# Optimization experiments

Hardware: AMD Instinct MI355X
Metric: run time of the kernel (lower is better)

The kernel has to match this reference:

```python
import jax, jax.numpy as jnp
import numpy as np

EPS = 1e-5

def binarize(x):
    # straight-through-estimator sign binarization (identity gradient),
    # matching the torch .data-mutation trick in BinarizeConv2d/BinarizeLinear
    return x + jax.lax.stop_gradient(jnp.sign(x) - x)

def conv3x3(x, w, b):
    # NCHW conv, stride 1, padding 1, binarized weights, float bias
    y = jax.lax.conv_general_dilated(x, binarize(w), window_strides=(1, 1),
                                     padding=((1, 1), (1, 1)),
                                     dimension_numbers=('NCHW', 'OIHW', 'NCHW'))
    return y + b[None, :, None, None]

def maxpool2(x):
    return jax.lax.reduce_window(x, -jnp.inf, jax.lax.max,
                                 (1, 1, 2, 2), (1, 1, 2, 2), 'VALID')

def bn2d(x, g, b):
    # training-mode batchnorm (batch statistics)
    m = jnp.mean(x, axis=(0, 2, 3), keepdims=True)
    v = jnp.var(x, axis=(0, 2, 3), keepdims=True)
    return (x - m) * jax.lax.rsqrt(v + EPS) * g[None, :, None, None] + b[None, :, None, None]

def bn1d(x, g, b):
    m = jnp.mean(x, axis=0)
    v = jnp.var(x, axis=0)
    return (x - m) * jax.lax.rsqrt(v + EPS) * g + b

def htanh(x):
    return jnp.clip(x, -1.0, 1.0)


def setup_inputs() -> dict:
    key = jax.random.key(0)
    ks = jax.random.split(key, 16)
    B = 1024
    inp = {
        'x':   jax.random.normal(ks[0], (B, 1, 28, 28), jnp.float32),
        'w1':  jax.random.normal(ks[1], (48, 1, 3, 3), jnp.float32) * 0.1,
        'b1':  jnp.zeros((48,), jnp.float32),
        'g1':  jnp.ones((48,), jnp.float32),  'be1': jnp.zeros((48,), jnp.float32),
        'w2':  jax.random.normal(ks[2], (128, 48, 3, 3), jnp.float32) * 0.05,
        'b2':  jnp.zeros((128,), jnp.float32),
        'g2':  jnp.ones((128,), jnp.float32), 'be2': jnp.zeros((128,), jnp.float32),
        'w3':  jax.random.normal(ks[3], (256, 128, 3, 3), jnp.float32) * 0.03,
        'b3':  jnp.zeros((256,), jnp.float32),
        'g3':  jnp.ones((256,), jnp.float32), 'be3': jnp.zeros((256,), jnp.float32),
        'wf1': jax.random.normal(ks[4], (2048, 256 * 7 * 7), jnp.float32) * 0.01,
        'bf1': jnp.zeros((2048,), jnp.float32),
        'g4':  jnp.ones((2048,), jnp.float32), 'be4': jnp.zeros((2048,), jnp.float32),
        'wf2': jax.random.normal(ks[5], (10, 2048), jnp.float32) * 0.02,
        'bf2': jnp.zeros((10,), jnp.float32),
    }
    return inp


def reference(x, w1, b1, g1, be1, w2, b2, g2, be2, w3, b3, g3, be3,
              wf1, bf1, g4, be4, wf2, bf2):
    # features
    h = conv3x3(binarize(x), w1, b1)          # [B,48,28,28] (input binarized: C=1 != 3)
    h = maxpool2(h)                            # [B,48,14,14]
    h = htanh(bn2d(h, g1, be1))
    h = conv3x3(binarize(h), w2, b2)          # [B,128,14,14]
    h = htanh(bn2d(h, g2, be2))
    h = conv3x3(binarize(h), w3, b3)          # [B,256,14,14]
    h = maxpool2(h)                            # [B,256,7,7]
    h = htanh(bn2d(h, g3, be3))
    # classifier
    h = h.reshape(-1, 256 * 7 * 7)
    h = binarize(h) @ binarize(wf1).T + bf1    # [B,2048]
    h = htanh(bn1d(h, g4, be4))
    # Dropout(0.5) is identity in eval mode
    h = h @ wf2.T + bf2                        # [B,10]
    return jax.nn.log_softmax(h, axis=1)
```

## Files before the change

### kernel.cpp

```cpp
#include <hip/hip_runtime.h>
#include <math.h>

typedef __attribute__((ext_vector_type(8))) short short8;
typedef __attribute__((ext_vector_type(4))) float f32x4;
typedef unsigned short ushort_t;

#define B_    1024
#define EPSV  1e-5

__device__ __forceinline__ float sgn(float v){ return (v>0.f)?1.f:((v<0.f)?-1.f:0.f); }
__device__ __forceinline__ ushort_t sgnbits(float v){ return (v>0.f)?(ushort_t)0x3F80:((v<0.f)?(ushort_t)0xBF80:(ushort_t)0); }

#define SWZW(o,c) ( ((o)<<6) ^ ((((c) ^ ((o)&7)) & 7) << 4) )
#define SWZF(o,c) ( ((o)<<7) + ((((c) ^ ((o)&7)) & 7) << 4) )

__global__ __launch_bounds__(256) void k_conv1_pool(const float* __restrict__ x,
                                                    const float* __restrict__ w1,
                                                    float* __restrict__ p1){
  int idx = blockIdx.x*256 + threadIdx.x;
  if (idx >= B_*196*64) return;
  int c = idx & 63;
  int p = (idx >> 6) % 196;
  int b = (idx >> 6) / 196;
  if (c >= 48){ p1[idx] = 0.f; return; }
  int y = p/14, xq = p - y*14;
  const float* xb = x + (size_t)b*784;
  float w[9];
#pragma unroll
  for (int k=0;k<9;k++) w[k] = sgn(w1[c*9+k]);
  float sx[4][4];
#pragma unroll
  for (int dy=0; dy<4; dy++){
    int iy = 2*y-1+dy;
#pragma unroll
    for (int dx=0; dx<4; dx++){
      int ix = 2*xq-1+dx;
      sx[dy][dx] = (iy>=0 && iy<28 && ix>=0 && ix<28) ? sgn(xb[iy*28+ix]) : 0.f;
    }
  }
  float best = -1e30f;
#pragma unroll
  for (int py=0;py<2;py++)
#pragma unroll
    for (int px=0;px<2;px++){
      float acc = 0.f;
#pragma unroll
      for (int ky=0;ky<3;ky++)
#pragma unroll
        for (int kx=0;kx<3;kx++)
          acc += sx[py+ky][px+kx]*w[ky*3+kx];
      best = fmaxf(best, acc);
    }
  p1[idx] = best;
}

__global__ __launch_bounds__(256) void k_stats_cl64(const float* __restrict__ src,
                                                    double* __restrict__ sum,
                                                    double* __restrict__ sumsq,
                                                    long rows){
  int c = threadIdx.x & 63, sl = threadIdx.x >> 6;
  double a=0.0, q=0.0;
  long stride = (long)gridDim.y*4;
  for (long r = (long)blockIdx.y*4 + sl; r < rows; r += stride){
    double v = (double)src[r*64 + c];
    a += v; q += v*v;
  }
  __shared__ double sA[256], sQd[256];
  sA[threadIdx.x]=a; sQd[threadIdx.x]=q;
  __syncthreads();
  if (threadIdx.x < 64){
    a = sA[threadIdx.x] + sA[threadIdx.x+64] + sA[threadIdx.x+128] + sA[threadIdx.x+192];
    q = sQd[threadIdx.x] + sQd[threadIdx.x+64] + sQd[threadIdx.x+128] + sQd[threadIdx.x+192];
    atomicAdd(&sum[c], a); atomicAdd(&sumsq[c], q);
  }
}

__global__ __launch_bounds__(256) void k_reduce_stats(const float* __restrict__ pS,
                                                      const float* __restrict__ pQ,
                                                      double* __restrict__ sum,
                                                      double* __restrict__ sumsq,
                                                      int C, int nPart){
  int c = blockIdx.x*256 + threadIdx.x;
  if (c >= C) return;
  int per = (nPart + gridDim.y - 1)/gridDim.y;
  int p0 = blockIdx.y*per, p1 = p0+per; if (p1 > nPart) p1 = nPart;
  double a=0.0, q=0.0;
  for (int p = p0; p < p1; ++p){
    a += (double)pS[(size_t)p*C + c];
    q += (double)pQ[(size_t)p*C + c];
  }
  atomicAdd(&sum[c], a); atomicAdd(&sumsq[c], q);
}

__global__ void k_bnparams(const double* __restrict__ sum, const double* __restrict__ sumsq,
                           const float* __restrict__ g, const float* __restrict__ be,
                           float* __restrict__ scale, float* __restrict__ shift,
                           int C, int validC, double invN){
  int c = blockIdx.x*blockDim.x + threadIdx.x;
  if (c >= C) return;
  if (c >= validC){ scale[c]=0.f; shift[c]=0.f; return; }
  double m   = sum[c]*invN;
  double var = sumsq[c]*invN - m*m;
  double s   = (double)g[c] / sqrt(var + EPSV);
  scale[c] = (float)s;
  shift[c] = (float)((double)be[c] - m*s);
}

__global__ __launch_bounds__(256) void k_norm_sign(const float* __restrict__ src,
                                                   ushort_t* __restrict__ dst,
                                                   const float* __restrict__ scale,
                                                   const float* __restrict__ shift,
                                                   int C, int S, int total){
  int i = blockIdx.x*256 + threadIdx.x;
  if (i >= total) return;
  int c = (i / S) % C;
  float v = fmaf(src[i], scale[c], shift[c]);
  dst[i] = sgnbits(v);
}

__global__ __launch_bounds__(256) void k_norm_htanh(float* __restrict__ buf,
                                                    const float* __restrict__ scale,
                                                    const float* __restrict__ shift,
                                                    int C, int total){
  int i = blockIdx.x*256 + threadIdx.x;
  if (i >= total) return;
  int c = i % C;
  float v = fmaf(buf[i], scale[c], shift[c]);
  buf[i] = fminf(fmaxf(v,-1.f),1.f);
}

__global__ __launch_bounds__(256) void k_prep_w2(const float* __restrict__ w2, ushort_t* __restrict__ out){
  int idx = blockIdx.x*256 + threadIdx.x;
  if (idx >= 128*576) return;
  int oc = idx / 576, r = idx - oc*576;
  int kk = r >> 6, ic = r & 63;
  out[idx] = (ic < 48) ? sgnbits(w2[oc*432 + ic*9 + kk]) : (ushort_t)0;
}
__global__ __launch_bounds__(256) void k_prep_w3(const float* __restrict__ w3, ushort_t* __restrict__ out){
  int idx = blockIdx.x*256 + threadIdx.x;
  if (idx >= 256*1152) return;
  int oc = idx / 1152, r = idx - oc*1152;
  int kk = r >> 7, ic = r & 127;
  out[idx] = sgnbits(w3[oc*1152 + ic*9 + kk]);
}
__global__ __launch_bounds__(256) void k_prep_wf1(const float* __restrict__ wf1, ushort_t* __restrict__ out){
  int idx = blockIdx.x*256 + threadIdx.x;
  if (idx >= 2048*12544/4) return;
  const float4 v = *reinterpret_cast<const float4*>(&wf1[(size_t)idx*4]);
  ushort4 o;
  o.x = sgnbits(v.x); o.y = sgnbits(v.y); o.z = sgnbits(v.z); o.w = sgnbits(v.w);
  *reinterpret_cast<ushort4*>(&out[(size_t)idx*4]) = o;
}

__global__ __launch_bounds__(256,2) void k_conv2_mfma(const ushort_t* __restrict__ a1,
                                                      const ushort_t* __restrict__ w2b,
                                                      float* __restrict__ c2,
                                                      float* __restrict__ pS,
                                                      float* __restrict__ pQ){
  __shared__ ushort_t sIn[256*64];
  __shared__ char     sWb[2][8192];
  __shared__ float    sRS[128], sRQ[128];
  int b = blockIdx.x, tid = threadIdx.x;
  {
    const uint4* src4 = reinterpret_cast<const uint4*>(a1 + (size_t)b*196*64);
    for (int i = tid; i < 2048; i += 256){
      int px = i >> 3, ch = i & 7;
      int py = px >> 4, pxx = px & 15;
      uint4 v = make_uint4(0u,0u,0u,0u);
      if (py>=1 && py<=14 && pxx>=1 && pxx<=14)
        v = src4[((py-1)*14 + (pxx-1))*8 + ch];
      *reinterpret_cast<uint4*>(&sIn[px*64 + ((ch ^ (px & 7))<<3)]) = v;
    }
  }
  if (tid < 128){ sRS[tid]=0.f; sRQ[tid]=0.f; }
  const uint4* gW = reinterpret_cast<const uint4*>(w2b);
  int cS = tid & 3, rS = (tid >> 2)*2;
  {
    uint4 v0 = gW[(size_t)rS*72 + cS];
    uint4 v1 = gW[(size_t)(rS+1)*72 + cS];
    *reinterpret_cast<uint4*>(&sWb[0][SWZW(rS,  cS)]) = v0;
    *reinterpret_cast<uint4*>(&sWb[0][SWZW(rS+1,cS)]) = v1;
  }
  __syncthreads();
  int lane = tid & 63, wave = tid >> 6;
  int rA = lane & 15, kch = lane >> 4;
  f32x4 acc[4][8];
#pragma unroll
  for (int t=0;t<4;t++)
#pragma unroll
    for (int n=0;n<8;n++) acc[t][n] = (f32x4){0.f,0.f,0.f,0.f};

  for (int s = 0; s < 18; ++s){
    int cur = s & 1;
    uint4 w0, w1;
    if (s < 17){
      w0 = gW[(size_t)rS*72 + (s+1)*4 + cS];
      w1 = gW[(size_t)(rS+1)*72 + (s+1)*4 + cS];
    }
    short8 bF[8];
#pragma unroll
    for (int n=0;n<8;n++){
      int o = n*16 + rA;
      bF[n] = *reinterpret_cast<const short8*>(&sWb[cur][SWZW(o, kch)]);
    }
    int kk9 = s >> 1;
    int ky = kk9/3, kx = kk9 - ky*3;
    int chbase = ((s & 1) << 2) + kch;
#pragma unroll
    for (int t=0;t<4;t++){
      int m = t*4 + wave;
      if (m < 13){
        int r = m*16 + rA;
        int rc = r < 196 ? r : 195;
        int y = rc/14, x = rc - y*14;
        int px = (y+ky)*16 + (x+kx);
        short8 aF = *reinterpret_cast<const short8*>(&sIn[px*64 + ((chbase ^ (px&7))<<3)]);
#pragma unroll
        for (int n=0;n<8;n++)
          acc[t][n] = __builtin_amdgcn_mfma_f32_16x16x32_bf16(aF, bF[n], acc[t][n], 0,0,0);
      }
    }
    if (s < 17){
      *reinterpret_cast<uint4*>(&sWb[cur^1][SWZW(rS,  cS)]) = w0;
      *reinterpret_cast<uint4*>(&sWb[cur^1][SWZW(rS+1,cS)]) = w1;
    }
    __syncthreads();
  }
  int colL = lane & 15, rg = lane >> 4;
  float csum[8], csq[8];
#pragma unroll
  for (int n=0;n<8;n++){ csum[n]=0.f; csq[n]=0.f; }
#pragma unroll
  for (int t=0;t<4;t++){
    int m = t*4 + wave;
    if (m < 13){
#pragma unroll
      for (int n=0;n<8;n++)
#pragma unroll
        for (int j=0;j<4;j++){
          int r = m*16 + rg*4 + j;
          if (r < 196){
            float v = acc[t][n][j];
            c2[((size_t)b*196 + r)*128 + n*16 + colL] = v;
            csum[n] += v; csq[n] += v*v;
          }
        }
    }
  }
#pragma unroll
  for (int n=0;n<8;n++){
    float a = csum[n], q = csq[n];
    a += __shfl_down(a,32); a += __shfl_down(a,16);
    q += __shfl_down(q,32); q += __shfl_down(q,16);
    if (rg == 0){
      atomicAdd(&sRS[n*16+colL], a);
      atomicAdd(&sRQ[n*16+colL], q);
    }
  }
  __syncthreads();
  if (tid < 128){
    pS[(size_t)b*128 + tid] = sRS[tid];
    pQ[(size_t)b*128 + tid] = sRQ[tid];
  }
}

__global__ __launch_bounds__(256,2) void k_conv3_mfma_pool(const ushort_t* __restrict__ a2,
                                                           const ushort_t* __restrict__ w3b,
                                                           float* __restrict__ p3,
                                                           float* __restrict__ pS,
                                                           float* __restrict__ pQ){
  __shared__ ushort_t sIn[256*64];
  __shared__ char     sWb[2][8192];
  __shared__ float    sS[32], sQ[32];
  int ocb = blockIdx.x*128;
  int b   = blockIdx.y;
  int tid = threadIdx.x;
  const uint4* src4 = reinterpret_cast<const uint4*>(a2 + (size_t)b*196*128);
  for (int i = tid; i < 2048; i += 256){
    int px = i >> 3, ch = i & 7;
    int py = px >> 4, pxx = px & 15;
    uint4 v = make_uint4(0u,0u,0u,0u);
    if (py>=1 && py<=14 && pxx>=1 && pxx<=14)
      v = src4[((py-1)*14 + (pxx-1))*16 + ch];
    *reinterpret_cast<uint4*>(&sIn[px*64 + ((ch ^ (px & 7))<<3)]) = v;
  }
  const uint4* gW = reinterpret_cast<const uint4*>(w3b);
  int cS = tid & 3, rS = (tid >> 2)*2;
  {
    uint4 v0 = gW[(size_t)(ocb+rS)*144 + cS];
    uint4 v1 = gW[(size_t)(ocb+rS+1)*144 + cS];
    *reinterpret_cast<uint4*>(&sWb[0][SWZW(rS,  cS)]) = v0;
    *reinterpret_cast<uint4*>(&sWb[0][SWZW(rS+1,cS)]) = v1;
  }
  __syncthreads();
  int lane = tid & 63, wave = tid >> 6;
  int rA = lane & 15, kch = lane >> 4;
  f32x4 acc[4][8];
#pragma unroll
  for (int t=0;t<4;t++)
#pragma unroll
    for (int n=0;n<8;n++) acc[t][n] = (f32x4){0.f,0.f,0.f,0.f};

  for (int s = 0; s < 36; ++s){
    int cur = s & 1;
    uint4 w0, w1;
    if (s < 35){
      int s1 = s+1; int h1 = (s1 >= 18); int sl1 = s1 - h1*18;
      int wofs = (sl1>>1)*16 + h1*8 + (sl1&1)*4;
      w0 = gW[(size_t)(ocb+rS)*144 + wofs + cS];
      w1 = gW[(size_t)(ocb+rS+1)*144 + wofs + cS];
    }
    short8 bF[8];
#pragma unroll
    for (int n=0;n<8;n++){
      int o = n*16 + rA;
      bF[n] = *reinterpret_cast<const short8*>(&sWb[cur][SWZW(o, kch)]);
    }
    int h = (s >= 18); int sloc = s - h*18;
    int kk9 = sloc >> 1;
    int ky = kk9/3, kx = kk9 - ky*3;
    int chbase = ((sloc & 1) << 2) + kch;
#pragma unroll
    for (int t=0;t<4;t++){
      int m = t*4 + wave;
      if (m < 13){
        int r = m*16 + rA;
        int rc = r < 196 ? r : 195;
        int y = rc/14, x = rc - y*14;
        int px = (y+ky)*16 + (x+kx);
        short8 aF = *reinterpret_cast<const short8*>(&sIn[px*64 + ((chbase ^ (px&7))<<3)]);
#pragma unroll
        for (int n=0;n<8;n++)
          acc[t][n] = __builtin_amdgcn_mfma_f32_16x16x32_bf16(aF, bF[n], acc[t][n], 0,0,0);
      }
    }
    if (s < 35){
      *reinterpret_cast<uint4*>(&sWb[cur^1][SWZW(rS,  cS)]) = w0;
      *reinterpret_cast<uint4*>(&sWb[cur^1][SWZW(rS+1,cS)]) = w1;
    }
    if (s == 17){
      __syncthreads();
      for (int i = tid; i < 2048; i += 256){
        int px = i >> 3, ch = i & 7;
        int py = px >> 4, pxx = px & 15;
        uint4 v = make_uint4(0u,0u,0u,0u);
        if (py>=1 && py<=14 && pxx>=1 && pxx<=14)
          v = src4[((py-1)*14 + (pxx-1))*16 + 8 + ch];
        *reinterpret_cast<uint4*>(&sIn[px*64 + ((ch ^ (px & 7))<<3)]) = v;
      }
      __syncthreads();
    } else {
      __syncthreads();
    }
  }
  float* sPool = reinterpret_cast<float*>(sIn);
  int colL = lane & 15, rg = lane >> 4;
  for (int q = 0; q < 4; ++q){
    __syncthreads();
#pragma unroll
    for (int t=0;t<4;t++){
      int m = t*4 + wave;
      if (m < 13){
#pragma unroll
        for (int nl=0;nl<2;nl++){
          int n = q*2 + nl;
#pragma unroll
          for (int j=0;j<4;j++){
            int r = m*16 + rg*4 + j;
            if (r < 196) sPool[(nl*16+colL)*197 + r] = acc[t][n][j];
          }
        }
      }
    }
    if (tid < 32){ sS[tid]=0.f; sQ[tid]=0.f; }
    __syncthreads();
    for (int i = tid; i < 32*49; i += 256){
      int oc = i/49, cell = i - oc*49;
      int cy = cell/7, cx = cell - cy*7;
      const float* rp = &sPool[oc*197 + cy*28 + cx*2];
      float v = fmaxf(fmaxf(rp[0],rp[1]), fmaxf(rp[14],rp[15]));
      p3[((size_t)b*256 + ocb + q*32 + oc)*49 + cell] = v;
      atomicAdd(&sS[oc], v); atomicAdd(&sQ[oc], v*v);
    }
    __syncthreads();
    if (tid < 32){
      pS[(size_t)b*256 + ocb + q*32 + tid] = sS[tid];
      pQ[(size_t)b*256 + ocb + q*32 + tid] = sQ[tid];
    }
  }
}

__global__ __launch_bounds__(256,2) void k_fc1_mfma(const ushort_t* __restrict__ A,
                                                    const ushort_t* __restrict__ Bw,
                                                    float* __restrict__ f1,
                                                    float* __restrict__ pS,
                                                    float* __restrict__ pQ){
  __shared__ char As[2][8192];
  __shared__ char Bs[2][16384];
  __shared__ float sCS[128], sCQ[128];
  int id = blockIdx.x;
  int bm = (id & 15) << 6, bn = (id >> 4) << 7;
  int tid = threadIdx.x;
  int cS = tid & 7;
  int rS = tid >> 3;
  const uint4* gA = reinterpret_cast<const uint4*>(A);
  const uint4* gB = reinterpret_cast<const uint4*>(Bw);
  {
    *reinterpret_cast<uint4*>(&As[0][SWZF(rS,   cS)]) = gA[(size_t)(bm+rS   )*1568 + cS];
    *reinterpret_cast<uint4*>(&As[0][SWZF(rS+32,cS)]) = gA[(size_t)(bm+rS+32)*1568 + cS];
#pragma unroll
    for (int j=0;j<4;j++)
      *reinterpret_cast<uint4*>(&Bs[0][SWZF(rS+j*32,cS)]) = gB[(size_t)(bn+rS+j*32)*1568 + cS];
  }
  if (tid < 128){ sCS[tid]=0.f; sCQ[tid]=0.f; }
  __syncthreads();
  int lane = tid & 63, wave = tid >> 6;
  int rA = lane & 15, kch = lane >> 4;
  int wm = wave & 1, wn = wave >> 1;
  f32x4 acc[2][4];
#pragma unroll
  for (int i=0;i<2;i++)
#pragma unroll
    for (int n=0;n<4;n++) acc[i][n] = (f32x4){0.f,0.f,0.f,0.f};

  for (int s = 0; s < 196; ++s){
    int cur = s & 1;
    uint4 pa0, pa1, pb[4];
    if (s < 195){
      size_t k0 = (size_t)(s+1)*8 + cS;
      pa0 = gA[(size_t)(bm+rS   )*1568 + k0];
      pa1 = gA[(size_t)(bm+rS+32)*1568 + k0];
#pragma unroll
      for (int j=0;j<4;j++)
        pb[j] = gB[(size_t)(bn+rS+j*32)*1568 + k0];
    }
#pragma unroll
    for (int u = 0; u < 2; ++u){
      short8 aF[2], bF[4];
#pragma unroll
      for (int i=0;i<2;i++){
        int ro = wm*32 + i*16 + rA;
        aF[i] = *reinterpret_cast<const short8*>(&As[cur][SWZF(ro, u*4+kch)]);
      }
#pragma unroll
      for (int n=0;n<4;n++){
        int co = wn*64 + n*16 + rA;
        bF[n] = *reinterpret_cast<const short8*>(&Bs[cur][SWZF(co, u*4+kch)]);
      }
#pragma unroll
      for (int i=0;i<2;i++)
#pragma unroll
        for (int n=0;n<4;n++)
          acc[i][n] = __builtin_amdgcn_mfma_f32_16x16x32_bf16(aF[i], bF[n], acc[i][n], 0,0,0);
    }
    if (s < 195){
      *reinterpret_cast<uint4*>(&As[cur^1][SWZF(rS,   cS)]) = pa0;
      *reinterpret_cast<uint4*>(&As[cur^1][SWZF(rS+32,cS)]) = pa1;
#pragma unroll
      for (int j=0;j<4;j++)
        *reinterpret_cast<uint4*>(&Bs[cur^1][SWZF(rS+j*32,cS)]) = pb[j];
    }
    __syncthreads();
  }
  int colL = lane & 15, rg = lane >> 4;
#pragma unroll
  for (int n=0;n<4;n++){
    float ls = 0.f, lq = 0.f;
#pragma unroll
    for (int i=0;i<2;i++)
#pragma unroll
      for (int j=0;j<4;j++){
        int r = bm + wm*32 + i*16 + rg*4 + j;
        float v = acc[i][n][j];
        f1[(size_t)r*2048 + bn + wn*64 + n*16 + colL] = v;
        ls += v; lq += v*v;
      }
    ls += __shfl_down(ls,32); ls += __shfl_down(ls,16);
    lq += __shfl_down(lq,32); lq += __shfl_down(lq,16);
    if (rg == 0){
      atomicAdd(&sCS[wn*64 + n*16 + colL], ls);
      atomicAdd(&sCQ[wn*64 + n*16 + colL], lq);
    }
  }
  __syncthreads();
  if (tid < 128){
    pS[(size_t)(id&15)*2048 + bn + tid] = sCS[tid];
    pQ[(size_t)(id&15)*2048 + bn + tid] = sCQ[tid];
  }
}

__global__ __launch_bounds__(256) void k_fc2_lsm(const float* __restrict__ h,
                                                 const float* __restrict__ W,
                                                 const float* __restrict__ bias,
                                                 float* __restrict__ out){
  int b = blockIdx.x;
  const float* hb = h + (size_t)b*2048;
  float acc[10];
#pragma unroll
  for (int o=0;o<10;o++) acc[o]=0.f;
  for (int k=threadIdx.x; k<2048; k+=256){
    float v = hb[k];
#pragma unroll
    for (int o=0;o<10;o++) acc[o] += v*W[o*2048+k];
  }
  __shared__ float red[4][10];
  int wv = threadIdx.x>>6, lanev = threadIdx.x&63;
#pragma unroll
  for (int o=0;o<10;o++){
    float r = acc[o];
    for (int off=32; off>0; off>>=1) r += __shfl_down(r, off);
    if (lanev==0) red[wv][o]=r;
  }
  __syncthreads();
  if (threadIdx.x==0){
    float lg[10], mx=-1e30f;
#pragma unroll
    for (int o=0;o<10;o++){ lg[o]=red[0][o]+red[1][o]+red[2][o]+red[3][o]+bias[o]; mx=fmaxf(mx,lg[o]); }
    float se=0.f;
#pragma unroll
    for (int o=0;o<10;o++) se += expf(lg[o]-mx);
    float lse = mx + logf(se);
#pragma unroll
    for (int o=0;o<10;o++) out[(size_t)b*10+o] = lg[o]-lse;
  }
}

extern "C" void kernel_launch(void* const* d_in, const int* in_sizes, int n_in,
                              void* d_out, int out_size, void* d_ws, size_t ws_size,
                              hipStream_t stream){
  (void)in_sizes; (void)n_in; (void)out_size; (void)ws_size;
  const float* x   = (const float*)d_in[0];
  const float* w1  = (const float*)d_in[1];
  const float* g1  = (const float*)d_in[3];
  const float* be1 = (const float*)d_in[4];
  const float* w2  = (const float*)d_in[5];
  const float* g2  = (const float*)d_in[7];
  const float* be2 = (const float*)d_in[8];
  const float* w3  = (const float*)d_in[9];
  const float* g3  = (const float*)d_in[11];
  const float* be3 = (const float*)d_in[12];
  const float* wf1 = (const float*)d_in[13];
  const float* g4  = (const float*)d_in[15];
  const float* be4 = (const float*)d_in[16];
  const float* wf2 = (const float*)d_in[17];
  const float* bf2 = (const float*)d_in[18];
  float* out = (float*)d_out;

  char* W = (char*)d_ws;
  double* sum   = (double*)W;
  double* sumsq = sum + 2048;
  float*  scale = (float*)(W + 32768);
  float*  shift = scale + 2048;
  float*    p1   = (float*)   (W + 65536);
  float*    c2   = (float*)   (W + 65536);
  float*    p3   = (float*)   (W + 65536);
  float*    f1   = (float*)   (W + 65536);
  ushort_t* a3   = (ushort_t*)(W + 51445760);
  ushort_t* wf1b = (ushort_t*)(W + 77135872);
  ushort_t* a1   = (ushort_t*)(W + 102825984);
  ushort_t* w2b  = (ushort_t*)(W + 128516096);
  ushort_t* a2   = (ushort_t*)(W + 128663552);
  ushort_t* w3b  = (ushort_t*)(W + 180043776);
  float*    pS2  = (float*)   (W + 180633600);
  float*    pQ2  = pS2 + 131072;
  float*    pS3  = pQ2 + 131072;
  float*    pQ3  = pS3 + 262144;
  float*    pSF  = pQ3 + 262144;
  float*    pQF  = pSF + 32768;

  k_conv1_pool<<<50176, 256, 0, stream>>>(x, w1, p1);
  hipMemsetAsync(sum, 0, 32768, stream);
  k_stats_cl64<<<dim3(1,128), 256, 0, stream>>>(p1, sum, sumsq, 200704L);
  k_bnparams<<<1, 256, 0, stream>>>(sum, sumsq, g1, be1, scale, shift, 64, 48, 1.0/200704.0);
  k_norm_sign<<<50176, 256, 0, stream>>>(p1, a1, scale, shift, 64, 1, 12845056);
  k_prep_w2<<<288, 256, 0, stream>>>(w2, w2b);
  k_prep_w3<<<1152, 256, 0, stream>>>(w3, w3b);
  k_conv2_mfma<<<1024, 256, 0, stream>>>(a1, w2b, c2, pS2, pQ2);
  hipMemsetAsync(sum, 0, 32768, stream);
  k_reduce_stats<<<dim3(1,32), 256, 0, stream>>>(pS2, pQ2, sum, sumsq, 128, 1024);
  k_bnparams<<<1, 256, 0, stream>>>(sum, sumsq, g2, be2, scale, shift, 128, 128, 1.0/200704.0);
  k_norm_sign<<<100352, 256, 0, stream>>>(c2, a2, scale, shift, 128, 1, 25690112);
  k_prep_wf1<<<25088, 256, 0, stream>>>(wf1, wf1b);
  k_conv3_mfma_pool<<<dim3(2, B_), 256, 0, stream>>>(a2, w3b, p3, pS3, pQ3);
  hipMemsetAsync(sum, 0, 32768, stream);
  k_reduce_stats<<<dim3(1,32), 256, 0, stream>>>(pS3, pQ3, sum, sumsq, 256, 1024);
  k_bnparams<<<1, 256, 0, stream>>>(sum, sumsq, g3, be3, scale, shift, 256, 256, 1.0/50176.0);
  k_norm_sign<<<50176, 256, 0, stream>>>(p3, a3, scale, shift, 256, 49, 12845056);
  k_fc1_mfma<<<256, 256, 0, stream>>>(a3, wf1b, f1, pSF, pQF);
  hipMemsetAsync(sum, 0, 32768, stream);
  k_reduce_stats<<<dim3(8,1), 256, 0, stream>>>(pSF, pQF, sum, sumsq, 2048, 16);
  k_bnparams<<<8, 256, 0, stream>>>(sum, sumsq, g4, be4, scale, shift, 2048, 2048, 1.0/1024.0);
  k_norm_htanh<<<8192, 256, 0, stream>>>(f1, scale, shift, 2048, 2097152);
  k_fc2_lsm<<<B_, 256, 0, stream>>>(f1, wf2, bf2, out);
}
```

Baseline: 1.077 ms.

## Split conv2/conv3 output channels across blocks and stream weights from global memory

Conv2 and conv3 now split output channels into 64-wide slices across a second grid dimension, doubling the block count. Weight fragments are loaded directly from global/L2 into registers with a two-slot register prefetch instead of going through shared-memory double buffering, which removes the per-step barriers. Conv3 keeps all 128 input channels resident in shared memory (64KB) and does the pool/stats epilogue in one pass with shuffle reductions. In exchange, input tiles are reloaded once per channel slice, weight loads rely on cache hits, and the larger shared memory footprint may cut occupancy.

```diff
diff --git a/kernel.cpp b/kernel.cpp
--- a/kernel.cpp
+++ b/kernel.cpp
@@ -10,9 +10,6 @@
 
 __device__ __forceinline__ float sgn(float v){ return (v>0.f)?1.f:((v<0.f)?-1.f:0.f); }
 __device__ __forceinline__ ushort_t sgnbits(float v){ return (v>0.f)?(ushort_t)0x3F80:((v<0.f)?(ushort_t)0xBF80:(ushort_t)0); }
-
-#define SWZW(o,c) ( ((o)<<6) ^ ((((c) ^ ((o)&7)) & 7) << 4) )
-#define SWZF(o,c) ( ((o)<<7) + ((((c) ^ ((o)&7)) & 7) << 4) )
 
 __global__ __launch_bounds__(256) void k_conv1_pool(const float* __restrict__ x,
                                                     const float* __restrict__ w1,
@@ -158,9 +155,10 @@
                                                       float* __restrict__ pS,
                                                       float* __restrict__ pQ){
   __shared__ ushort_t sIn[256*64];
-  __shared__ char     sWb[2][8192];
-  __shared__ float    sRS[128], sRQ[128];
-  int b = blockIdx.x, tid = threadIdx.x;
+  __shared__ float sRS[64], sRQ[64];
+  int ocb = blockIdx.x*64;
+  int b   = blockIdx.y;
+  int tid = threadIdx.x;
   {
     const uint4* src4 = reinterpret_cast<const uint4*>(a1 + (size_t)b*196*64);
     for (int i = tid; i < 2048; i += 256){
@@ -172,95 +170,79 @@
       *reinterpret_cast<uint4*>(&sIn[px*64 + ((ch ^ (px & 7))<<3)]) = v;
     }
   }
-  if (tid < 128){ sRS[tid]=0.f; sRQ[tid]=0.f; }
-  const uint4* gW = reinterpret_cast<const uint4*>(w2b);
-  int cS = tid & 3, rS = (tid >> 2)*2;
-  {
-    uint4 v0 = gW[(size_t)rS*72 + cS];
-    uint4 v1 = gW[(size_t)(rS+1)*72 + cS];
-    *reinterpret_cast<uint4*>(&sWb[0][SWZW(rS,  cS)]) = v0;
-    *reinterpret_cast<uint4*>(&sWb[0][SWZW(rS+1,cS)]) = v1;
-  }
+  if (tid < 64){ sRS[tid]=0.f; sRQ[tid]=0.f; }
   __syncthreads();
   int lane = tid & 63, wave = tid >> 6;
   int rA = lane & 15, kch = lane >> 4;
-  f32x4 acc[4][8];
+  const uint4* gW = reinterpret_cast<const uint4*>(w2b);
+  size_t wrow[4];
+#pragma unroll
+  for (int n=0;n<4;n++) wrow[n] = (size_t)(ocb + n*16 + rA)*72 + kch;
+  f32x4 acc[4][4];
 #pragma unroll
   for (int t=0;t<4;t++)
 #pragma unroll
-    for (int n=0;n<8;n++) acc[t][n] = (f32x4){0.f,0.f,0.f,0.f};
-
-  for (int s = 0; s < 18; ++s){
-    int cur = s & 1;
-    uint4 w0, w1;
-    if (s < 17){
-      w0 = gW[(size_t)rS*72 + (s+1)*4 + cS];
-      w1 = gW[(size_t)(rS+1)*72 + (s+1)*4 + cS];
-    }
-    short8 bF[8];
-#pragma unroll
-    for (int n=0;n<8;n++){
-      int o = n*16 + rA;
-      bF[n] = *reinterpret_cast<const short8*>(&sWb[cur][SWZW(o, kch)]);
-    }
-    int kk9 = s >> 1;
-    int ky = kk9/3, kx = kk9 - ky*3;
-    int chbase = ((s & 1) << 2) + kch;
+    for (int n=0;n<4;n++) acc[t][n] = (f32x4){0.f,0.f,0.f,0.f};
+
+  uint4 bA[4], bB[4];
+#pragma unroll
+  for (int n=0;n<4;n++){ bA[n] = gW[wrow[n]]; bB[n] = gW[wrow[n] + 4]; }
+
+#define C2_MSTEP(S, BSLOT, PRE) { \
+    short8 bF[4]; \
+    _Pragma("unroll") for (int n=0;n<4;n++) bF[n] = *reinterpret_cast<short8*>(&BSLOT[n]); \
+    if ((S)+2 < 18){ _Pragma("unroll") for (int n=0;n<4;n++) BSLOT[n] = gW[wrow[n] + ((S)+2)*4]; } \
+    int kk9 = (S) >> 1; int ky = kk9/3, kx = kk9 - ky*3; \
+    int chbase = (((S) & 1) << 2) + kch; \
+    _Pragma("unroll") for (int t=0;t<4;t++){ \
+      int m = t*4 + wave; \
+      if (m < 13){ \
+        int r = m*16 + rA; int rc = r < 196 ? r : 195; \
+        int y = rc/14, xx = rc - y*14; \
+        int px = (y+ky)*16 + (xx+kx); \
+        short8 aF = *reinterpret_cast<const short8*>(&sIn[px*64 + ((chbase ^ (px&7))<<3)]); \
+        _Pragma("unroll") for (int n=0;n<4;n++) \
+          acc[t][n] = __builtin_amdgcn_mfma_f32_16x16x32_bf16(aF, bF[n], acc[t][n], 0,0,0); \
+      } \
+    } }
+
+  for (int sp = 0; sp < 9; ++sp){
+    int s0 = sp*2;
+    C2_MSTEP(s0,   bA, )
+    C2_MSTEP(s0+1, bB, )
+  }
+#undef C2_MSTEP
+
+  int colL = lane & 15, rg = lane >> 4;
+#pragma unroll
+  for (int n=0;n<4;n++){
+    float csum = 0.f, csq = 0.f;
 #pragma unroll
     for (int t=0;t<4;t++){
       int m = t*4 + wave;
       if (m < 13){
-        int r = m*16 + rA;
-        int rc = r < 196 ? r : 195;
-        int y = rc/14, x = rc - y*14;
-        int px = (y+ky)*16 + (x+kx);
-        short8 aF = *reinterpret_cast<const short8*>(&sIn[px*64 + ((chbase ^ (px&7))<<3)]);
-#pragma unroll
-        for (int n=0;n<8;n++)
-          acc[t][n] = __builtin_amdgcn_mfma_f32_16x16x32_bf16(aF, bF[n], acc[t][n], 0,0,0);
-      }
-    }
-    if (s < 17){
-      *reinterpret_cast<uint4*>(&sWb[cur^1][SWZW(rS,  cS)]) = w0;
-      *reinterpret_cast<uint4*>(&sWb[cur^1][SWZW(rS+1,cS)]) = w1;
-    }
-    __syncthreads();
-  }
-  int colL = lane & 15, rg = lane >> 4;
-  float csum[8], csq[8];
-#pragma unroll
-  for (int n=0;n<8;n++){ csum[n]=0.f; csq[n]=0.f; }
-#pragma unroll
-  for (int t=0;t<4;t++){
-    int m = t*4 + wave;
-    if (m < 13){
-#pragma unroll
-      for (int n=0;n<8;n++)
 #pragma unroll
         for (int j=0;j<4;j++){
           int r = m*16 + rg*4 + j;
           if (r < 196){
             float v = acc[t][n][j];
-            c2[((size_t)b*196 + r)*128 + n*16 + colL] = v;
-            csum[n] += v; csq[n] += v*v;
+            c2[((size_t)b*196 + r)*128 + ocb + n*16 + colL] = v;
+            csum += v; csq += v*v;
           }
         }
-    }
-  }
-#pragma unroll
-  for (int n=0;n<8;n++){
-    float a = csum[n], q = csq[n];
-    a += __shfl_down(a,32); a += __shfl_down(a,16);
-    q += __shfl_down(q,32); q += __shfl_down(q,16);
+      }
+    }
+    csum += __shfl_down(csum,32); csum += __shfl_down(csum,16);
+    csq  += __shfl_down(csq, 32); csq  += __shfl_down(csq, 16);
     if (rg == 0){
-      atomicAdd(&sRS[n*16+colL], a);
-      atomicAdd(&sRQ[n*16+colL], q);
-    }
-  }
-  __syncthreads();
-  if (tid < 128){
-    pS[(size_t)b*128 + tid] = sRS[tid];
-    pQ[(size_t)b*128 + tid] = sRQ[tid];
+      atomicAdd(&sRS[n*16+colL], csum);
+      atomicAdd(&sRQ[n*16+colL], csq);
+    }
+  }
+  __syncthreads();
+  if (tid < 64){
+    pS[(size_t)b*128 + ocb + tid] = sRS[tid];
+    pQ[(size_t)b*128 + ocb + tid] = sRQ[tid];
   }
 }
 
@@ -269,127 +251,105 @@
                                                            float* __restrict__ p3,
                                                            float* __restrict__ pS,
                                                            float* __restrict__ pQ){
-  __shared__ ushort_t sIn[256*64];
-  __shared__ char     sWb[2][8192];
-  __shared__ float    sS[32], sQ[32];
-  int ocb = blockIdx.x*128;
+  __shared__ ushort_t sIn[256*128];
+  int ocb = blockIdx.x*64;
   int b   = blockIdx.y;
   int tid = threadIdx.x;
-  const uint4* src4 = reinterpret_cast<const uint4*>(a2 + (size_t)b*196*128);
-  for (int i = tid; i < 2048; i += 256){
-    int px = i >> 3, ch = i & 7;
-    int py = px >> 4, pxx = px & 15;
-    uint4 v = make_uint4(0u,0u,0u,0u);
-    if (py>=1 && py<=14 && pxx>=1 && pxx<=14)
-      v = src4[((py-1)*14 + (pxx-1))*16 + ch];
-    *reinterpret_cast<uint4*>(&sIn[px*64 + ((ch ^ (px & 7))<<3)]) = v;
-  }
-  const uint4* gW = reinterpret_cast<const uint4*>(w3b);
-  int cS = tid & 3, rS = (tid >> 2)*2;
   {
-    uint4 v0 = gW[(size_t)(ocb+rS)*144 + cS];
-    uint4 v1 = gW[(size_t)(ocb+rS+1)*144 + cS];
-    *reinterpret_cast<uint4*>(&sWb[0][SWZW(rS,  cS)]) = v0;
-    *reinterpret_cast<uint4*>(&sWb[0][SWZW(rS+1,cS)]) = v1;
+    const uint4* src4 = reinterpret_cast<const uint4*>(a2 + (size_t)b*196*128);
+    for (int i = tid; i < 4096; i += 256){
+      int px = i >> 4, ch = i & 15;
+      int py = px >> 4, pxx = px & 15;
+      uint4 v = make_uint4(0u,0u,0u,0u);
+      if (py>=1 && py<=14 && pxx>=1 && pxx<=14)
+        v = src4[((py-1)*14 + (pxx-1))*16 + ch];
+      *reinterpret_cast<uint4*>(&sIn[px*128 + ((ch ^ (px & 15))<<3)]) = v;
+    }
   }
   __syncthreads();
   int lane = tid & 63, wave = tid >> 6;
   int rA = lane & 15, kch = lane >> 4;
-  f32x4 acc[4][8];
+  const uint4* gW = reinterpret_cast<const uint4*>(w3b);
+  size_t wrow[4];
+#pragma unroll
+  for (int n=0;n<4;n++) wrow[n] = (size_t)(ocb + n*16 + rA)*144 + kch;
+  f32x4 acc[4][4];
 #pragma unroll
   for (int t=0;t<4;t++)
 #pragma unroll
-    for (int n=0;n<8;n++) acc[t][n] = (f32x4){0.f,0.f,0.f,0.f};
-
-  for (int s = 0; s < 36; ++s){
-    int cur = s & 1;
-    uint4 w0, w1;
-    if (s < 35){
-      int s1 = s+1; int h1 = (s1 >= 18); int sl1 = s1 - h1*18;
-      int wofs = (sl1>>1)*16 + h1*8 + (sl1&1)*4;
-      w0 = gW[(size_t)(ocb+rS)*144 + wofs + cS];
-      w1 = gW[(size_t)(ocb+rS+1)*144 + wofs + cS];
-    }
-    short8 bF[8];
-#pragma unroll
-    for (int n=0;n<8;n++){
-      int o = n*16 + rA;
-      bF[n] = *reinterpret_cast<const short8*>(&sWb[cur][SWZW(o, kch)]);
-    }
-    int h = (s >= 18); int sloc = s - h*18;
-    int kk9 = sloc >> 1;
-    int ky = kk9/3, kx = kk9 - ky*3;
-    int chbase = ((sloc & 1) << 2) + kch;
-#pragma unroll
-    for (int t=0;t<4;t++){
-      int m = t*4 + wave;
-      if (m < 13){
-        int r = m*16 + rA;
-        int rc = r < 196 ? r : 195;
-        int y = rc/14, x = rc - y*14;
-        int px = (y+ky)*16 + (x+kx);
-        short8 aF = *reinterpret_cast<const short8*>(&sIn[px*64 + ((chbase ^ (px&7))<<3)]);
-#pragma unroll
-        for (int n=0;n<8;n++)
-          acc[t][n] = __builtin_amdgcn_mfma_f32_16x16x32_bf16(aF, bF[n], acc[t][n], 0,0,0);
-      }
-    }
-    if (s < 35){
-      *reinterpret_cast<uint4*>(&sWb[cur^1][SWZW(rS,  cS)]) = w0;
-      *reinterpret_cast<uint4*>(&sWb[cur^1][SWZW(rS+1,cS)]) = w1;
-    }
-    if (s == 17){
-      __syncthreads();
-      for (int i = tid; i < 2048; i += 256){
-        int px = i >> 3, ch = i & 7;
-        int py = px >> 4, pxx = px & 15;
-        uint4 v = make_uint4(0u,0u,0u,0u);
-        if (py>=1 && py<=14 && pxx>=1 && pxx<=14)
-          v = src4[((py-1)*14 + (pxx-1))*16 + 8 + ch];
-        *reinterpret_cast<uint4*>(&sIn[px*64 + ((ch ^ (px & 7))<<3)]) = v;
-      }
-      __syncthreads();
-    } else {
-      __syncthreads();
-    }
-  }
+    for (int n=0;n<4;n++) acc[t][n] = (f32x4){0.f,0.f,0.f,0.f};
+
+  uint4 bA[4], bB[4];
+#pragma unroll
+  for (int n=0;n<4;n++){ bA[n] = gW[wrow[n]]; bB[n] = gW[wrow[n] + 4]; }
+
+#define C3_MSTEP(S, BSLOT) { \
+    short8 bF[4]; \
+    _Pragma("unroll") for (int n=0;n<4;n++) bF[n] = *reinterpret_cast<short8*>(&BSLOT[n]); \
+    if ((S)+2 < 36){ _Pragma("unroll") for (int n=0;n<4;n++) BSLOT[n] = gW[wrow[n] + ((S)+2)*4]; } \
+    int kk9 = (S) >> 2; int ky = kk9/3, kx = kk9 - ky*3; \
+    int chbase = (((S) & 3) << 2) + kch; \
+    _Pragma("unroll") for (int t=0;t<4;t++){ \
+      int m = t*4 + wave; \
+      if (m < 13){ \
+        int r = m*16 + rA; int rc = r < 196 ? r : 195; \
+        int y = rc/14, xx = rc - y*14; \
+        int px = (y+ky)*16 + (xx+kx); \
+        short8 aF = *reinterpret_cast<const short8*>(&sIn[px*128 + ((chbase ^ (px&15))<<3)]); \
+        _Pragma("unroll") for (int n=0;n<4;n++) \
+          acc[t][n] = __builtin_amdgcn_mfma_f32_16x16x32_bf16(aF, bF[n], acc[t][n], 0,0,0); \
+      } \
+    } }
+
+  for (int sp = 0; sp < 18; ++sp){
+    int s0 = sp*2;
+    C3_MSTEP(s0,   bA)
+    C3_MSTEP(s0+1, bB)
+  }
+#undef C3_MSTEP
+
+  __syncthreads();
   float* sPool = reinterpret_cast<float*>(sIn);
   int colL = lane & 15, rg = lane >> 4;
-  for (int q = 0; q < 4; ++q){
-    __syncthreads();
-#pragma unroll
-    for (int t=0;t<4;t++){
-      int m = t*4 + wave;
-      if (m < 13){
-#pragma unroll
-        for (int nl=0;nl<2;nl++){
-          int n = q*2 + nl;
-#pragma unroll
-          for (int j=0;j<4;j++){
-            int r = m*16 + rg*4 + j;
-            if (r < 196) sPool[(nl*16+colL)*197 + r] = acc[t][n][j];
-          }
+#pragma unroll
+  for (int t=0;t<4;t++){
+    int m = t*4 + wave;
+    if (m < 13){
+#pragma unroll
+      for (int n=0;n<4;n++)
+#pragma unroll
+        for (int j=0;j<4;j++){
+          int r = m*16 + rg*4 + j;
+          if (r < 196) sPool[(n*16+colL)*213 + r] = acc[t][n][j];
         }
+    }
+  }
+  __syncthreads();
+  {
+    int oc = tid >> 2, part = tid & 3;
+    float ls = 0.f, lq = 0.f;
+    const float* rowp = &sPool[oc*213];
+    float* outp = &p3[((size_t)b*256 + ocb + oc)*49];
+    for (int ci = 0; ci < 13; ++ci){
+      int cell = part*13 + ci;
+      if (cell < 49){
+        int cy = cell/7, cx = cell - cy*7;
+        const float* rp = rowp + cy*28 + cx*2;
+        float v = fmaxf(fmaxf(rp[0],rp[1]), fmaxf(rp[14],rp[15]));
+        outp[cell] = v;
+        ls += v; lq += v*v;
       }
     }
-    if (tid < 32){ sS[tid]=0.f; sQ[tid]=0.f; }
-    __syncthreads();
-    for (int i = tid; i < 32*49; i += 256){
-      int oc = i/49, cell = i - oc*49;
-      int cy = cell/7, cx = cell - cy*7;
-      const float* rp = &sPool[oc*197 + cy*28 + cx*2];
-      float v = fmaxf(fmaxf(rp[0],rp[1]), fmaxf(rp[14],rp[15]));
-      p3[((size_t)b*256 + ocb + q*32 + oc)*49 + cell] = v;
-      atomicAdd(&sS[oc], v); atomicAdd(&sQ[oc], v*v);
-    }
-    __syncthreads();
-    if (tid < 32){
-      pS[(size_t)b*256 + ocb + q*32 + tid] = sS[tid];
-      pQ[(size_t)b*256 + ocb + q*32 + tid] = sQ[tid];
-    }
-  }
-}
-
+    ls += __shfl_down(ls,1); ls += __shfl_down(ls,2);
+    lq += __shfl_down(lq,1); lq += __shfl_down(lq,2);
+    if (part == 0){
+      pS[(size_t)b*256 + ocb + oc] = ls;
+      pQ[(size_t)b*256 + ocb + oc] = lq;
+    }
+  }
+}
+
+#define SWZF(o,c) ( ((o)<<7) + ((((c) ^ ((o)&7)) & 7) << 4) )
 __global__ __launch_bounds__(256,2) void k_fc1_mfma(const ushort_t* __restrict__ A,
                                                     const ushort_t* __restrict__ Bw,
                                                     float* __restrict__ f1,
@@ -575,13 +535,13 @@
   k_norm_sign<<<50176, 256, 0, stream>>>(p1, a1, scale, shift, 64, 1, 12845056);
   k_prep_w2<<<288, 256, 0, stream>>>(w2, w2b);
   k_prep_w3<<<1152, 256, 0, stream>>>(w3, w3b);
-  k_conv2_mfma<<<1024, 256, 0, stream>>>(a1, w2b, c2, pS2, pQ2);
+  k_conv2_mfma<<<dim3(2, B_), 256, 0, stream>>>(a1, w2b, c2, pS2, pQ2);
   hipMemsetAsync(sum, 0, 32768, stream);
   k_reduce_stats<<<dim3(1,32), 256, 0, stream>>>(pS2, pQ2, sum, sumsq, 128, 1024);
   k_bnparams<<<1, 256, 0, stream>>>(sum, sumsq, g2, be2, scale, shift, 128, 128, 1.0/200704.0);
   k_norm_sign<<<100352, 256, 0, stream>>>(c2, a2, scale, shift, 128, 1, 25690112);
   k_prep_wf1<<<25088, 256, 0, stream>>>(wf1, wf1b);
-  k_conv3_mfma_pool<<<dim3(2, B_), 256, 0, stream>>>(a2, w3b, p3, pS3, pQ3);
+  k_conv3_mfma_pool<<<dim3(4, B_), 256, 0, stream>>>(a2, w3b, p3, pS3, pQ3);
   hipMemsetAsync(sum, 0, 32768, stream);
   k_reduce_stats<<<dim3(1,32), 256, 0, stream>>>(pS3, pQ3, sum, sumsq, 256, 1024);
   k_bnparams<<<1, 256, 0, stream>>>(sum, sumsq, g3, be3, scale, shift, 256, 256, 1.0/50176.0);
```

Measured after the change: 1.110 ms. 3.0% more time.
